# Optimization experiments

Measured on AMD Instinct MI355X. Metric: run time of the kernel, lower is better.

Reference implementation:

```python
import jax, jax.numpy as jnp
import numpy as np

B, N, D = 4, 2048, 512
H, DH = 8, 64  # heads, dim_head; inner_dim = H*DH = 512
SCALE = DH ** -0.5


def setup_inputs() -> dict:
    key = jax.random.key(0)
    kx, kw = jax.random.split(key)
    x = jax.random.normal(kx, (B, N, D), dtype=jnp.float32)
    # torch Linear weight layout: [out_features=3*H*DH, in_features=D]
    W_qkv = jax.random.normal(kw, (3 * H * DH, D), dtype=jnp.float32) * 0.02
    return {"x": x, "W_qkv": W_qkv}


def reference(x, W_qkv):
    b, n, d = x.shape
    # qkv projection (no bias since qkv_bias=False)
    qkv = x @ W_qkv.T                                  # [b, n, 3*H*DH]
    qkv = qkv.reshape(b, n, 3, H, DH).transpose(2, 0, 3, 1, 4)  # [3, b, H, n, DH]
    q, k, v = qkv[0], qkv[1], qkv[2]
    # shifted query: q_cross[t] = q[t-1] for t>=1, q_cross[0] = q[0]
    q_cross = jnp.concatenate([q[:, :, :1, :], q[:, :, :-1, :]], axis=2)
    scores = jnp.einsum("bhqd,bhkd->bhqk", q_cross * SCALE, k)  # [b, H, n, n]
    attn = jax.nn.softmax(scores, axis=-1)
    out = jnp.einsum("bhqk,bhkd->bhqd", attn, v)       # [b, H, n, DH]
    out = out.transpose(0, 2, 1, 3).reshape(b, n, H * DH)
    # to_out is Dropout(0.0) -> identity in eval / p=0
    return out
```

## Files before the change

kernel.cpp:

```cpp
#include <hip/hip_runtime.h>
#include <hip/hip_bf16.h>
#include <stdint.h>

typedef __bf16 bf16_t;
typedef float floatx4 __attribute__((ext_vector_type(4)));
typedef __bf16 bf16x8 __attribute__((ext_vector_type(8)));
typedef __bf16 bf16x4 __attribute__((ext_vector_type(4)));

#define QSCALE 0.1803368801111204f

__device__ __forceinline__ void gl2lds16(const bf16_t* g, bf16_t* l) {
    __builtin_amdgcn_global_load_lds(
        (const __attribute__((address_space(1))) unsigned int*)g,
        (__attribute__((address_space(3))) unsigned int*)l,
        16, 0, 0);
}

__global__ __launch_bounds__(256) void convert_kernel(const float* __restrict__ x,
                                                      bf16_t* __restrict__ xb,
                                                      const float* __restrict__ w,
                                                      bf16_t* __restrict__ wb,
                                                      int nx4) {
    int i = blockIdx.x * 256 + threadIdx.x;
    const float* in; bf16_t* out; int j;
    if (i < nx4) { in = x; out = xb; j = i; }
    else         { in = w; out = wb; j = i - nx4; }
    float4 v = ((const float4*)in)[j];
    bf16x4 o;
    o.x = (bf16_t)v.x; o.y = (bf16_t)v.y; o.z = (bf16_t)v.z; o.w = (bf16_t)v.w;
    ((bf16x4*)out)[j] = o;
}

__global__ __launch_bounds__(256) void qkv_gemm(const bf16_t* __restrict__ X,
                                                const bf16_t* __restrict__ W,
                                                bf16_t* __restrict__ Q,
                                                bf16_t* __restrict__ K,
                                                bf16_t* __restrict__ Vt)
{
    __shared__ bf16_t As[128 * 64];
    __shared__ bf16_t Bs[128 * 64];

    const int tid  = threadIdx.x;
    const int wave = tid >> 6;
    const int lane = tid & 63;
    const int quad = lane >> 4;
    const int lrow = lane & 15;
    const int t7g  = lrow & 7;
    const int bm0 = blockIdx.x * 128;
    const int bn0 = blockIdx.y * 128;
    const int mw = (wave >> 1) * 64;
    const int nw = (wave & 1) * 64;
    const int wbase = tid & 192;

    floatx4 acc[4][4];
#pragma unroll
    for (int i = 0; i < 4; i++)
#pragma unroll
        for (int j = 0; j < 4; j++) acc[i][j] = (floatx4)0.0f;

#pragma unroll 1
    for (int kb = 0; kb < 8; ++kb) {
        const int k0 = kb * 64;
        __syncthreads();
#pragma unroll
        for (int r = 0; r < 4; ++r) {
            int c = r * 256 + tid;
            int row = c >> 3, kc = c & 7;
            int skc = kc ^ (row & 7);
            gl2lds16(X + (size_t)(bm0 + row) * 512 + k0 + skc * 8,
                     As + (size_t)(r * 256 + wbase) * 8);
        }
#pragma unroll
        for (int r = 0; r < 4; ++r) {
            int c = r * 256 + tid;
            int row = c >> 3, kc = c & 7;
            int skc = kc ^ (row & 7);
            gl2lds16(W + (size_t)(bn0 + row) * 512 + k0 + skc * 8,
                     Bs + (size_t)(r * 256 + wbase) * 8);
        }
        __syncthreads();
#pragma unroll
        for (int ks = 0; ks < 2; ++ks) {
            bf16x8 af[4], bfr[4];
#pragma unroll
            for (int mi = 0; mi < 4; mi++)
                af[mi] = *(const bf16x8*)(As + (mw + mi * 16 + lrow) * 64 + (((ks * 4 + quad) ^ t7g) << 3));
#pragma unroll
            for (int ni = 0; ni < 4; ni++)
                bfr[ni] = *(const bf16x8*)(Bs + (nw + ni * 16 + lrow) * 64 + (((ks * 4 + quad) ^ t7g) << 3));
#pragma unroll
            for (int mi = 0; mi < 4; mi++)
#pragma unroll
                for (int ni = 0; ni < 4; ni++)
                    acc[mi][ni] = __builtin_amdgcn_mfma_f32_16x16x32_bf16(af[mi], bfr[ni], acc[mi][ni], 0, 0, 0);
        }
    }

#pragma unroll
    for (int mi = 0; mi < 4; mi++) {
        int mbase = bm0 + mw + mi * 16 + quad * 4;
        int b = mbase >> 11, n = mbase & 2047;
#pragma unroll
        for (int ni = 0; ni < 4; ni++) {
            int o = bn0 + nw + ni * 16 + lrow;
            int s  = o >> 9;
            int h  = (o >> 6) & 7;
            int dh = o & 63;
            int bh = b * 8 + h;
            if (s == 2) {
                bf16x4 pv;
#pragma unroll
                for (int r = 0; r < 4; r++) pv[r] = (bf16_t)acc[mi][ni][r];
                *(bf16x4*)(Vt + ((size_t)bh * 64 + dh) * 2048 + n) = pv;
            } else if (s == 0) {
#pragma unroll
                for (int r = 0; r < 4; r++)
                    Q[((size_t)bh * 2048 + n + r) * 64 + dh] = (bf16_t)(acc[mi][ni][r] * QSCALE);
            } else {
#pragma unroll
                for (int r = 0; r < 4; r++)
                    K[((size_t)bh * 2048 + n + r) * 64 + dh] = (bf16_t)acc[mi][ni][r];
            }
        }
    }
}

__device__ __forceinline__ void stage_tile(const bf16_t* __restrict__ kb,
                                           const bf16_t* __restrict__ vb,
                                           int kt, bf16_t* ksbuf, bf16_t* vsbuf,
                                           int wave, int lane) {
#pragma unroll
    for (int part = 0; part < 2; ++part) {
        int ch  = part * 256 + wave * 64 + lane;
        int row = ch >> 3, cc = ch & 7;
        int scc = cc ^ (row & 7);
        bf16_t* ldst = ksbuf + (size_t)(part * 256 + wave * 64) * 8;
        gl2lds16(kb + ((size_t)(kt * 64 + row)) * 64 + scc * 8, ldst);
        bf16_t* ldst2 = vsbuf + (size_t)(part * 256 + wave * 64) * 8;
        gl2lds16(vb + (size_t)row * 2048 + kt * 64 + scc * 8, ldst2);
    }
}

__global__ __launch_bounds__(256) void flash_attn(const bf16_t* __restrict__ Q,
                                                  const bf16_t* __restrict__ K,
                                                  const bf16_t* __restrict__ Vt,
                                                  float* __restrict__ Out)
{
    __shared__ bf16_t Ks[2][64 * 64];
    __shared__ bf16_t Vs[2][64 * 64];
    __shared__ bf16_t Ps[4][16 * 64];

    const int tid  = threadIdx.x;
    const int wave = tid >> 6;
    const int lane = tid & 63;
    const int quad = lane >> 4;
    const int c    = lane & 15;
    const int t7   = c & 7;
    const int qt = blockIdx.x;
    const int bh = blockIdx.y;
    const int b = bh >> 3, h = bh & 7;

    int qg  = qt * 64 + wave * 16 + c;
    int src = (qg == 0) ? 0 : qg - 1;
    const bf16_t* qbase = Q + ((size_t)bh * 2048 + src) * 64;
    bf16x8 qf0 = *(const bf16x8*)(qbase + quad * 8);
    bf16x8 qf1 = *(const bf16x8*)(qbase + 32 + quad * 8);

    floatx4 o[4];
#pragma unroll
    for (int i = 0; i < 4; i++) o[i] = (floatx4)0.0f;
    float lacc[4] = {0.f, 0.f, 0.f, 0.f};

    const bf16_t* kb = K + ((size_t)bh * 2048) * 64;
    const bf16_t* vb = Vt + ((size_t)bh * 64) * 2048;
    bf16_t* pw = Ps[wave];

    stage_tile(kb, vb, 0, Ks[0], Vs[0], wave, lane);

#pragma unroll 1
    for (int kt = 0; kt < 32; ++kt) {
        const int buf = kt & 1;
        __syncthreads();
        if (kt < 31)
            stage_tile(kb, vb, kt + 1, Ks[buf ^ 1], Vs[buf ^ 1], wave, lane);

        const bf16_t* ks = Ks[buf];
        const bf16_t* vs = Vs[buf];

        floatx4 s[4];
#pragma unroll
        for (int sub = 0; sub < 4; ++sub) {
            const bf16_t* krow = ks + (sub * 16 + c) * 64;
            bf16x8 kf0 = *(const bf16x8*)(krow + ((quad ^ t7) << 3));
            bf16x8 kf1 = *(const bf16x8*)(krow + (((4 + quad) ^ t7) << 3));
            floatx4 t = (floatx4)0.0f;
            t = __builtin_amdgcn_mfma_f32_16x16x32_bf16(qf0, kf0, t, 0, 0, 0);
            t = __builtin_amdgcn_mfma_f32_16x16x32_bf16(qf1, kf1, t, 0, 0, 0);
            s[sub] = t;
        }

#pragma unroll
        for (int sub = 0; sub < 4; ++sub)
#pragma unroll
            for (int r = 0; r < 4; r++) {
                float p = __builtin_amdgcn_exp2f(s[sub][r]);
                lacc[r] += p;
                int row  = quad * 4 + r;
                int col8 = sub * 2 + (c >> 3);
                pw[row * 64 + ((col8 ^ (row & 7)) << 3) + t7] = (bf16_t)p;
            }

#pragma unroll
        for (int ki = 0; ki < 2; ++ki) {
            bf16x8 pf = *(const bf16x8*)(pw + c * 64 + (((ki * 4 + quad) ^ t7) << 3));
#pragma unroll
            for (int sub = 0; sub < 4; ++sub) {
                const bf16_t* vrow = vs + (sub * 16 + c) * 64;
                bf16x8 vf = *(const bf16x8*)(vrow + (((ki * 4 + quad) ^ t7) << 3));
                o[sub] = __builtin_amdgcn_mfma_f32_16x16x32_bf16(pf, vf, o[sub], 0, 0, 0);
            }
        }
    }

#pragma unroll
    for (int r = 0; r < 4; r++)
#pragma unroll
        for (int d = 1; d < 16; d <<= 1)
            lacc[r] += __shfl_xor(lacc[r], d, 64);

    int n0 = qt * 64 + wave * 16 + quad * 4;
    float* ob = Out + (size_t)b * 2048 * 512 + (size_t)h * 64;
#pragma unroll
    for (int r = 0; r < 4; r++) {
        float inv = 1.0f / lacc[r];
        float* orow = ob + (size_t)(n0 + r) * 512;
#pragma unroll
        for (int sub = 0; sub < 4; ++sub)
            orow[sub * 16 + c] = o[sub][r] * inv;
    }
}

extern "C" void kernel_launch(void* const* d_in, const int* in_sizes, int n_in,
                              void* d_out, int out_size, void* d_ws, size_t ws_size,
                              hipStream_t stream) {
    const float* x = (const float*)d_in[0];
    const float* w = (const float*)d_in[1];
    float* out = (float*)d_out;

    char* ws = (char*)d_ws;
    bf16_t* xb = (bf16_t*)(ws);
    bf16_t* wb = (bf16_t*)(ws + 8388608);
    bf16_t* q  = (bf16_t*)(ws + 9961472);
    bf16_t* k  = (bf16_t*)(ws + 18350080);
    bf16_t* vt = (bf16_t*)(ws + 26738688);

    convert_kernel<<<4864, 256, 0, stream>>>(x, xb, w, wb, 1048576);
    qkv_gemm<<<dim3(64, 12), 256, 0, stream>>>(xb, wb, q, k, vt);
    flash_attn<<<dim3(32, 32), 256, 0, stream>>>(q, k, vt, out);
}
```

Baseline: 155.9 us.

## Use two waves per block with 32 query rows each, reusing K/V fragments

The flash attention block drops from four waves of 16 query rows to two waves of 32 query rows. Each K and V fragment read from LDS now feeds two MFMAs, which halves LDS read traffic per unit of compute. The tile staging loop is adjusted for 128 threads, and s_setprio hints are added around the MFMA phases. In exchange there are fewer waves per block, more accumulator registers per thread, and more staging work per thread.

Result: no change. 158.1 us (+1.4%).

```diff
diff --git a/kernel.cpp b/kernel.cpp
--- a/kernel.cpp
+++ b/kernel.cpp
@@ -130,25 +130,25 @@
                                            int kt, bf16_t* ksbuf, bf16_t* vsbuf,
                                            int wave, int lane) {
 #pragma unroll
-    for (int part = 0; part < 2; ++part) {
-        int ch  = part * 256 + wave * 64 + lane;
+    for (int part = 0; part < 4; ++part) {
+        int ch  = part * 128 + wave * 64 + lane;
         int row = ch >> 3, cc = ch & 7;
         int scc = cc ^ (row & 7);
-        bf16_t* ldst = ksbuf + (size_t)(part * 256 + wave * 64) * 8;
+        bf16_t* ldst = ksbuf + (size_t)(part * 128 + wave * 64) * 8;
         gl2lds16(kb + ((size_t)(kt * 64 + row)) * 64 + scc * 8, ldst);
-        bf16_t* ldst2 = vsbuf + (size_t)(part * 256 + wave * 64) * 8;
+        bf16_t* ldst2 = vsbuf + (size_t)(part * 128 + wave * 64) * 8;
         gl2lds16(vb + (size_t)row * 2048 + kt * 64 + scc * 8, ldst2);
     }
 }
 
-__global__ __launch_bounds__(256) void flash_attn(const bf16_t* __restrict__ Q,
+__global__ __launch_bounds__(128) void flash_attn(const bf16_t* __restrict__ Q,
                                                   const bf16_t* __restrict__ K,
                                                   const bf16_t* __restrict__ Vt,
                                                   float* __restrict__ Out)
 {
     __shared__ bf16_t Ks[2][64 * 64];
     __shared__ bf16_t Vs[2][64 * 64];
-    __shared__ bf16_t Ps[4][16 * 64];
+    __shared__ bf16_t Ps[2][32 * 64];
 
     const int tid  = threadIdx.x;
     const int wave = tid >> 6;
@@ -160,16 +160,22 @@
     const int bh = blockIdx.y;
     const int b = bh >> 3, h = bh & 7;
 
-    int qg  = qt * 64 + wave * 16 + c;
-    int src = (qg == 0) ? 0 : qg - 1;
-    const bf16_t* qbase = Q + ((size_t)bh * 2048 + src) * 64;
-    bf16x8 qf0 = *(const bf16x8*)(qbase + quad * 8);
-    bf16x8 qf1 = *(const bf16x8*)(qbase + 32 + quad * 8);
-
-    floatx4 o[4];
-#pragma unroll
-    for (int i = 0; i < 4; i++) o[i] = (floatx4)0.0f;
-    float lacc[4] = {0.f, 0.f, 0.f, 0.f};
+    bf16x8 qf[2][2];
+#pragma unroll
+    for (int mt = 0; mt < 2; ++mt) {
+        int qg  = qt * 64 + wave * 32 + mt * 16 + c;
+        int src = (qg == 0) ? 0 : qg - 1;
+        const bf16_t* qbase = Q + ((size_t)bh * 2048 + src) * 64;
+        qf[mt][0] = *(const bf16x8*)(qbase + quad * 8);
+        qf[mt][1] = *(const bf16x8*)(qbase + 32 + quad * 8);
+    }
+
+    floatx4 o[2][4];
+#pragma unroll
+    for (int mt = 0; mt < 2; ++mt)
+#pragma unroll
+        for (int i = 0; i < 4; i++) o[mt][i] = (floatx4)0.0f;
+    float lacc[2][4] = {{0.f, 0.f, 0.f, 0.f}, {0.f, 0.f, 0.f, 0.f}};
 
     const bf16_t* kb = K + ((size_t)bh * 2048) * 64;
     const bf16_t* vb = Vt + ((size_t)bh * 64) * 2048;
@@ -187,56 +193,70 @@
         const bf16_t* ks = Ks[buf];
         const bf16_t* vs = Vs[buf];
 
-        floatx4 s[4];
+        floatx4 s[2][4];
+        __builtin_amdgcn_s_setprio(1);
 #pragma unroll
         for (int sub = 0; sub < 4; ++sub) {
             const bf16_t* krow = ks + (sub * 16 + c) * 64;
             bf16x8 kf0 = *(const bf16x8*)(krow + ((quad ^ t7) << 3));
             bf16x8 kf1 = *(const bf16x8*)(krow + (((4 + quad) ^ t7) << 3));
-            floatx4 t = (floatx4)0.0f;
-            t = __builtin_amdgcn_mfma_f32_16x16x32_bf16(qf0, kf0, t, 0, 0, 0);
-            t = __builtin_amdgcn_mfma_f32_16x16x32_bf16(qf1, kf1, t, 0, 0, 0);
-            s[sub] = t;
-        }
-
-#pragma unroll
-        for (int sub = 0; sub < 4; ++sub)
-#pragma unroll
-            for (int r = 0; r < 4; r++) {
-                float p = __builtin_amdgcn_exp2f(s[sub][r]);
-                lacc[r] += p;
-                int row  = quad * 4 + r;
-                int col8 = sub * 2 + (c >> 3);
-                pw[row * 64 + ((col8 ^ (row & 7)) << 3) + t7] = (bf16_t)p;
+#pragma unroll
+            for (int mt = 0; mt < 2; ++mt) {
+                floatx4 t = (floatx4)0.0f;
+                t = __builtin_amdgcn_mfma_f32_16x16x32_bf16(qf[mt][0], kf0, t, 0, 0, 0);
+                t = __builtin_amdgcn_mfma_f32_16x16x32_bf16(qf[mt][1], kf1, t, 0, 0, 0);
+                s[mt][sub] = t;
             }
-
+        }
+        __builtin_amdgcn_s_setprio(0);
+
+#pragma unroll
+        for (int mt = 0; mt < 2; ++mt)
+#pragma unroll
+            for (int sub = 0; sub < 4; ++sub)
+#pragma unroll
+                for (int r = 0; r < 4; r++) {
+                    float p = __builtin_amdgcn_exp2f(s[mt][sub][r]);
+                    lacc[mt][r] += p;
+                    int row  = mt * 16 + quad * 4 + r;
+                    int col8 = sub * 2 + (c >> 3);
+                    pw[row * 64 + ((col8 ^ (row & 7)) << 3) + t7] = (bf16_t)p;
+                }
+
+        __builtin_amdgcn_s_setprio(1);
 #pragma unroll
         for (int ki = 0; ki < 2; ++ki) {
-            bf16x8 pf = *(const bf16x8*)(pw + c * 64 + (((ki * 4 + quad) ^ t7) << 3));
+            bf16x8 pf0 = *(const bf16x8*)(pw + c * 64 + (((ki * 4 + quad) ^ t7) << 3));
+            bf16x8 pf1 = *(const bf16x8*)(pw + (16 + c) * 64 + (((ki * 4 + quad) ^ t7) << 3));
 #pragma unroll
             for (int sub = 0; sub < 4; ++sub) {
                 const bf16_t* vrow = vs + (sub * 16 + c) * 64;
                 bf16x8 vf = *(const bf16x8*)(vrow + (((ki * 4 + quad) ^ t7) << 3));
-                o[sub] = __builtin_amdgcn_mfma_f32_16x16x32_bf16(pf, vf, o[sub], 0, 0, 0);
+                o[0][sub] = __builtin_amdgcn_mfma_f32_16x16x32_bf16(pf0, vf, o[0][sub], 0, 0, 0);
+                o[1][sub] = __builtin_amdgcn_mfma_f32_16x16x32_bf16(pf1, vf, o[1][sub], 0, 0, 0);
             }
         }
-    }
-
-#pragma unroll
-    for (int r = 0; r < 4; r++)
-#pragma unroll
-        for (int d = 1; d < 16; d <<= 1)
-            lacc[r] += __shfl_xor(lacc[r], d, 64);
-
-    int n0 = qt * 64 + wave * 16 + quad * 4;
+        __builtin_amdgcn_s_setprio(0);
+    }
+
     float* ob = Out + (size_t)b * 2048 * 512 + (size_t)h * 64;
 #pragma unroll
-    for (int r = 0; r < 4; r++) {
-        float inv = 1.0f / lacc[r];
-        float* orow = ob + (size_t)(n0 + r) * 512;
-#pragma unroll
-        for (int sub = 0; sub < 4; ++sub)
-            orow[sub * 16 + c] = o[sub][r] * inv;
+    for (int mt = 0; mt < 2; ++mt) {
+#pragma unroll
+        for (int r = 0; r < 4; r++)
+#pragma unroll
+            for (int d = 1; d < 16; d <<= 1)
+                lacc[mt][r] += __shfl_xor(lacc[mt][r], d, 64);
+
+        int n0 = qt * 64 + wave * 32 + mt * 16 + quad * 4;
+#pragma unroll
+        for (int r = 0; r < 4; r++) {
+            float inv = 1.0f / lacc[mt][r];
+            float* orow = ob + (size_t)(n0 + r) * 512;
+#pragma unroll
+            for (int sub = 0; sub < 4; ++sub)
+                orow[sub * 16 + c] = o[mt][sub][r] * inv;
+        }
     }
 }
 
@@ -256,5 +276,5 @@
 
     convert_kernel<<<4864, 256, 0, stream>>>(x, xb, w, wb, 1048576);
     qkv_gemm<<<dim3(64, 12), 256, 0, stream>>>(xb, wb, q, k, vt);
-    flash_attn<<<dim3(32, 32), 256, 0, stream>>>(q, k, vt, out);
-}
+    flash_attn<<<dim3(32, 32), 128, 0, stream>>>(q, k, vt, out);
+}
```

## Restructure attention to 32x32 MFMA with key-split waves and register P

Applied to the files above, without the earlier changes.

Rewrites the flash attention kernel to use 32x32x16 MFMA tiles. S is computed transposed (K×Q) so the exp'd probabilities can be repacked into the PV operand in registers via permlane32_swap, removing the per-wave LDS round trip for P. Waves are split into query halves and key halves, and the two key-half partial outputs and row sums are combined through LDS at the end. It also adds block-index swizzling for cache locality, a manually unrolled double-buffer loop, s_setprio around MFMA groups, and occupancy launch bounds. The cost is an extra reduction phase and higher register pressure.

Result: faster. 147.2 us (-5.6%).

```diff
diff --git a/kernel.cpp b/kernel.cpp
--- a/kernel.cpp
+++ b/kernel.cpp
@@ -4,8 +4,10 @@
 
 typedef __bf16 bf16_t;
 typedef float floatx4 __attribute__((ext_vector_type(4)));
+typedef float floatx16 __attribute__((ext_vector_type(16)));
 typedef __bf16 bf16x8 __attribute__((ext_vector_type(8)));
 typedef __bf16 bf16x4 __attribute__((ext_vector_type(4)));
+typedef unsigned int uintx4 __attribute__((ext_vector_type(4)));
 
 #define QSCALE 0.1803368801111204f
 
@@ -14,6 +16,12 @@
         (const __attribute__((address_space(1))) unsigned int*)g,
         (__attribute__((address_space(3))) unsigned int*)l,
         16, 0, 0);
+}
+
+__device__ __forceinline__ unsigned pk2(float lo, float hi) {
+    unsigned short a = __builtin_bit_cast(unsigned short, (bf16_t)lo);
+    unsigned short b = __builtin_bit_cast(unsigned short, (bf16_t)hi);
+    return (unsigned)a | ((unsigned)b << 16);
 }
 
 __global__ __launch_bounds__(256) void convert_kernel(const float* __restrict__ x,
@@ -125,118 +133,179 @@
     }
 }
 
-__device__ __forceinline__ void stage_tile(const bf16_t* __restrict__ kb,
-                                           const bf16_t* __restrict__ vb,
-                                           int kt, bf16_t* ksbuf, bf16_t* vsbuf,
-                                           int wave, int lane) {
-#pragma unroll
-    for (int part = 0; part < 2; ++part) {
-        int ch  = part * 256 + wave * 64 + lane;
-        int row = ch >> 3, cc = ch & 7;
-        int scc = cc ^ (row & 7);
-        bf16_t* ldst = ksbuf + (size_t)(part * 256 + wave * 64) * 8;
-        gl2lds16(kb + ((size_t)(kt * 64 + row)) * 64 + scc * 8, ldst);
-        bf16_t* ldst2 = vsbuf + (size_t)(part * 256 + wave * 64) * 8;
-        gl2lds16(vb + (size_t)row * 2048 + kt * 64 + scc * 8, ldst2);
-    }
-}
-
-__global__ __launch_bounds__(256) void flash_attn(const bf16_t* __restrict__ Q,
-                                                  const bf16_t* __restrict__ K,
-                                                  const bf16_t* __restrict__ Vt,
-                                                  float* __restrict__ Out)
+__global__ __launch_bounds__(256, 4) void flash_attn(const bf16_t* __restrict__ Q,
+                                                     const bf16_t* __restrict__ K,
+                                                     const bf16_t* __restrict__ Vt,
+                                                     float* __restrict__ Out)
 {
     __shared__ bf16_t Ks[2][64 * 64];
     __shared__ bf16_t Vs[2][64 * 64];
-    __shared__ bf16_t Ps[4][16 * 64];
 
     const int tid  = threadIdx.x;
     const int wave = tid >> 6;
     const int lane = tid & 63;
-    const int quad = lane >> 4;
-    const int c    = lane & 15;
-    const int t7   = c & 7;
-    const int qt = blockIdx.x;
-    const int bh = blockIdx.y;
-    const int b = bh >> 3, h = bh & 7;
-
-    int qg  = qt * 64 + wave * 16 + c;
+    const int l31  = lane & 31;
+    const int h    = lane >> 5;
+    const int l7   = lane & 7;
+    const int qhalf = wave >> 1;
+    const int khalf = wave & 1;
+
+    int raw = blockIdx.x + (blockIdx.y << 5);
+    int swz = (raw & 7) * 128 + (raw >> 3);
+    const int qt = swz & 31;
+    const int bh = swz >> 5;
+    const int b = bh >> 3, hd = bh & 7;
+
+    int qg  = qt * 64 + qhalf * 32 + l31;
     int src = (qg == 0) ? 0 : qg - 1;
     const bf16_t* qbase = Q + ((size_t)bh * 2048 + src) * 64;
-    bf16x8 qf0 = *(const bf16x8*)(qbase + quad * 8);
-    bf16x8 qf1 = *(const bf16x8*)(qbase + 32 + quad * 8);
-
-    floatx4 o[4];
-#pragma unroll
-    for (int i = 0; i < 4; i++) o[i] = (floatx4)0.0f;
-    float lacc[4] = {0.f, 0.f, 0.f, 0.f};
+    bf16x8 qf0 = *(const bf16x8*)(qbase + 0 * 16 + h * 8);
+    bf16x8 qf1 = *(const bf16x8*)(qbase + 1 * 16 + h * 8);
+    bf16x8 qf2 = *(const bf16x8*)(qbase + 2 * 16 + h * 8);
+    bf16x8 qf3 = *(const bf16x8*)(qbase + 3 * 16 + h * 8);
+
+    floatx16 O0 = (floatx16)0.0f;
+    floatx16 O1 = (floatx16)0.0f;
+    float lacc = 0.0f;
 
     const bf16_t* kb = K + ((size_t)bh * 2048) * 64;
     const bf16_t* vb = Vt + ((size_t)bh * 64) * 2048;
-    bf16_t* pw = Ps[wave];
-
-    stage_tile(kb, vb, 0, Ks[0], Vs[0], wave, lane);
+
+    const int ch0 = wave * 64 + lane;
+    const int r0s = ch0 >> 3, c0s = (ch0 & 7) ^ (r0s & 7);
+    const int ch1 = 256 + ch0;
+    const int r1s = ch1 >> 3, c1s = (ch1 & 7) ^ (r1s & 7);
+    const bf16_t* gk0 = kb + r0s * 64 + c0s * 8;
+    const bf16_t* gk1 = kb + r1s * 64 + c1s * 8;
+    const bf16_t* gv0 = vb + (size_t)r0s * 2048 + c0s * 8;
+    const bf16_t* gv1 = vb + (size_t)r1s * 2048 + c1s * 8;
+    const int woff = wave * 512;
+
+    auto STAGE = [&](int bufI, int kt) {
+        gl2lds16(gk0 + (size_t)kt * 4096, Ks[bufI] + woff);
+        gl2lds16(gk1 + (size_t)kt * 4096, Ks[bufI] + 2048 + woff);
+        gl2lds16(gv0 + kt * 64, Vs[bufI] + woff);
+        gl2lds16(gv1 + kt * 64, Vs[bufI] + 2048 + woff);
+    };
+
+    const int krow = (khalf * 32 + l31) * 64;
+    const int koff0 = krow + (((0 * 2 + h) ^ l7) << 3);
+    const int koff1 = krow + (((1 * 2 + h) ^ l7) << 3);
+    const int koff2 = krow + (((2 * 2 + h) ^ l7) << 3);
+    const int koff3 = krow + (((3 * 2 + h) ^ l7) << 3);
+    const int vr0 = l31 * 64, vr1 = (l31 + 32) * 64;
+    const int voff00 = vr0 + (((khalf * 4 + 0 * 2 + h) ^ l7) << 3);
+    const int voff01 = vr0 + (((khalf * 4 + 1 * 2 + h) ^ l7) << 3);
+    const int voff10 = vr1 + (((khalf * 4 + 0 * 2 + h) ^ l7) << 3);
+    const int voff11 = vr1 + (((khalf * 4 + 1 * 2 + h) ^ l7) << 3);
+
+    auto COMPUTE = [&](const bf16_t* ks, const bf16_t* vs) {
+        floatx16 S = (floatx16)0.0f;
+        __builtin_amdgcn_s_setprio(1);
+        bf16x8 kf0 = *(const bf16x8*)(ks + koff0);
+        S = __builtin_amdgcn_mfma_f32_32x32x16_bf16(kf0, qf0, S, 0, 0, 0);
+        bf16x8 kf1 = *(const bf16x8*)(ks + koff1);
+        S = __builtin_amdgcn_mfma_f32_32x32x16_bf16(kf1, qf1, S, 0, 0, 0);
+        bf16x8 kf2 = *(const bf16x8*)(ks + koff2);
+        S = __builtin_amdgcn_mfma_f32_32x32x16_bf16(kf2, qf2, S, 0, 0, 0);
+        bf16x8 kf3 = *(const bf16x8*)(ks + koff3);
+        S = __builtin_amdgcn_mfma_f32_32x32x16_bf16(kf3, qf3, S, 0, 0, 0);
+        __builtin_amdgcn_s_setprio(0);
+
+        float pe[16];
+#pragma unroll
+        for (int r = 0; r < 16; ++r) {
+            float p = __builtin_amdgcn_exp2f(S[r]);
+            lacc += p;
+            pe[r] = p;
+        }
+        unsigned PA0 = pk2(pe[0],  pe[1]),  PA1 = pk2(pe[2],  pe[3]);
+        unsigned PB0 = pk2(pe[4],  pe[5]),  PB1 = pk2(pe[6],  pe[7]);
+        unsigned PC0 = pk2(pe[8],  pe[9]),  PC1 = pk2(pe[10], pe[11]);
+        unsigned PD0 = pk2(pe[12], pe[13]), PD1 = pk2(pe[14], pe[15]);
+        auto s0 = __builtin_amdgcn_permlane32_swap((int)PA0, (int)PB0, false, false);
+        auto s1 = __builtin_amdgcn_permlane32_swap((int)PA1, (int)PB1, false, false);
+        auto s2 = __builtin_amdgcn_permlane32_swap((int)PC0, (int)PD0, false, false);
+        auto s3 = __builtin_amdgcn_permlane32_swap((int)PC1, (int)PD1, false, false);
+        uintx4 f0, f1;
+        f0.x = (unsigned)s0[0]; f0.y = (unsigned)s1[0]; f0.z = (unsigned)s0[1]; f0.w = (unsigned)s1[1];
+        f1.x = (unsigned)s2[0]; f1.y = (unsigned)s3[0]; f1.z = (unsigned)s2[1]; f1.w = (unsigned)s3[1];
+        bf16x8 frag0 = __builtin_bit_cast(bf16x8, f0);
+        bf16x8 frag1 = __builtin_bit_cast(bf16x8, f1);
+
+        __builtin_amdgcn_s_setprio(1);
+        bf16x8 vf00 = *(const bf16x8*)(vs + voff00);
+        O0 = __builtin_amdgcn_mfma_f32_32x32x16_bf16(frag0, vf00, O0, 0, 0, 0);
+        bf16x8 vf01 = *(const bf16x8*)(vs + voff01);
+        O0 = __builtin_amdgcn_mfma_f32_32x32x16_bf16(frag1, vf01, O0, 0, 0, 0);
+        bf16x8 vf10 = *(const bf16x8*)(vs + voff10);
+        O1 = __builtin_amdgcn_mfma_f32_32x32x16_bf16(frag0, vf10, O1, 0, 0, 0);
+        bf16x8 vf11 = *(const bf16x8*)(vs + voff11);
+        O1 = __builtin_amdgcn_mfma_f32_32x32x16_bf16(frag1, vf11, O1, 0, 0, 0);
+        __builtin_amdgcn_s_setprio(0);
+    };
+
+    STAGE(0, 0);
 
 #pragma unroll 1
-    for (int kt = 0; kt < 32; ++kt) {
-        const int buf = kt & 1;
+    for (int j = 0; j < 16; ++j) {
         __syncthreads();
-        if (kt < 31)
-            stage_tile(kb, vb, kt + 1, Ks[buf ^ 1], Vs[buf ^ 1], wave, lane);
-
-        const bf16_t* ks = Ks[buf];
-        const bf16_t* vs = Vs[buf];
-
-        floatx4 s[4];
-#pragma unroll
-        for (int sub = 0; sub < 4; ++sub) {
-            const bf16_t* krow = ks + (sub * 16 + c) * 64;
-            bf16x8 kf0 = *(const bf16x8*)(krow + ((quad ^ t7) << 3));
-            bf16x8 kf1 = *(const bf16x8*)(krow + (((4 + quad) ^ t7) << 3));
-            floatx4 t = (floatx4)0.0f;
-            t = __builtin_amdgcn_mfma_f32_16x16x32_bf16(qf0, kf0, t, 0, 0, 0);
-            t = __builtin_amdgcn_mfma_f32_16x16x32_bf16(qf1, kf1, t, 0, 0, 0);
-            s[sub] = t;
-        }
-
-#pragma unroll
-        for (int sub = 0; sub < 4; ++sub)
-#pragma unroll
-            for (int r = 0; r < 4; r++) {
-                float p = __builtin_amdgcn_exp2f(s[sub][r]);
-                lacc[r] += p;
-                int row  = quad * 4 + r;
-                int col8 = sub * 2 + (c >> 3);
-                pw[row * 64 + ((col8 ^ (row & 7)) << 3) + t7] = (bf16_t)p;
-            }
-
-#pragma unroll
-        for (int ki = 0; ki < 2; ++ki) {
-            bf16x8 pf = *(const bf16x8*)(pw + c * 64 + (((ki * 4 + quad) ^ t7) << 3));
-#pragma unroll
-            for (int sub = 0; sub < 4; ++sub) {
-                const bf16_t* vrow = vs + (sub * 16 + c) * 64;
-                bf16x8 vf = *(const bf16x8*)(vrow + (((ki * 4 + quad) ^ t7) << 3));
-                o[sub] = __builtin_amdgcn_mfma_f32_16x16x32_bf16(pf, vf, o[sub], 0, 0, 0);
-            }
-        }
-    }
-
-#pragma unroll
-    for (int r = 0; r < 4; r++)
-#pragma unroll
-        for (int d = 1; d < 16; d <<= 1)
-            lacc[r] += __shfl_xor(lacc[r], d, 64);
-
-    int n0 = qt * 64 + wave * 16 + quad * 4;
-    float* ob = Out + (size_t)b * 2048 * 512 + (size_t)h * 64;
-#pragma unroll
-    for (int r = 0; r < 4; r++) {
-        float inv = 1.0f / lacc[r];
-        float* orow = ob + (size_t)(n0 + r) * 512;
-#pragma unroll
-        for (int sub = 0; sub < 4; ++sub)
-            orow[sub * 16 + c] = o[sub][r] * inv;
+        STAGE(1, 2 * j + 1);
+        COMPUTE(Ks[0], Vs[0]);
+        __syncthreads();
+        if (j < 15) STAGE(0, 2 * j + 2);
+        COMPUTE(Ks[1], Vs[1]);
+    }
+
+    lacc += __shfl_xor(lacc, 32, 64);
+
+    __syncthreads();
+    float* obuf = (float*)Ks;
+    float* lbuf = (float*)Vs;
+    const int obase = qhalf * 2048 + lane * 32;
+    if (khalf == 1) {
+#pragma unroll
+        for (int g = 0; g < 4; ++g) {
+            floatx4 v4;
+#pragma unroll
+            for (int e = 0; e < 4; ++e) v4[e] = O0[g * 4 + e];
+            *(floatx4*)(obuf + obase + (((0 * 4 + g) ^ l7) << 2)) = v4;
+        }
+#pragma unroll
+        for (int g = 0; g < 4; ++g) {
+            floatx4 v4;
+#pragma unroll
+            for (int e = 0; e < 4; ++e) v4[e] = O1[g * 4 + e];
+            *(floatx4*)(obuf + obase + (((1 * 4 + g) ^ l7) << 2)) = v4;
+        }
+        if (lane < 32) lbuf[qhalf * 32 + l31] = lacc;
+    }
+    __syncthreads();
+    if (khalf == 0) {
+#pragma unroll
+        for (int g = 0; g < 4; ++g) {
+            floatx4 v4 = *(const floatx4*)(obuf + obase + (((0 * 4 + g) ^ l7) << 2));
+#pragma unroll
+            for (int e = 0; e < 4; ++e) O0[g * 4 + e] += v4[e];
+        }
+#pragma unroll
+        for (int g = 0; g < 4; ++g) {
+            floatx4 v4 = *(const floatx4*)(obuf + obase + (((1 * 4 + g) ^ l7) << 2));
+#pragma unroll
+            for (int e = 0; e < 4; ++e) O1[g * 4 + e] += v4[e];
+        }
+        lacc += lbuf[qhalf * 32 + l31];
+
+        float* ob = Out + (size_t)b * 2048 * 512 + (size_t)hd * 64;
+#pragma unroll
+        for (int r = 0; r < 16; ++r) {
+            int qr = (r & 3) + 8 * (r >> 2) + 4 * h;
+            float lr = __shfl(lacc, qr, 64);
+            float inv = 1.0f / lr;
+            float* orow = ob + (size_t)(qt * 64 + qhalf * 32 + qr) * 512;
+            orow[l31]      = O0[r] * inv;
+            orow[32 + l31] = O1[r] * inv;
+        }
     }
 }
 
```
